# Performance work log

Hardware: AMD Instinct MI355X
Metric: run time of the kernel (lower is better)

Reference implementation:

```python
import jax, jax.numpy as jnp
import numpy as np

N = 8192      # num nodes (fea.shape[0])
IN = 512      # in_features (fea.shape[1])
H = 64        # nhidden
DEG = 32      # avg degree
E = N * DEG   # num edges


def setup_inputs() -> dict:
    key = jax.random.key(0)
    k1, k2, k3 = jax.random.split(key, 3)
    x = jax.random.normal(k1, (N, IN), dtype=jnp.float32)
    # glorot-uniform-scaled params (stored as [in, out] for x @ W)
    W = jax.random.uniform(k2, (IN, H), jnp.float32, -1.0, 1.0) * np.sqrt(6.0 / (IN + H))
    a = jax.random.uniform(k3, (2 * H, 1), jnp.float32, -1.0, 1.0) * np.sqrt(6.0 / (2 * H + 1))
    # structured edge list: no self-loops, no duplicate edges (matches nonzero of a
    # zero-diagonal adjacency; indexed-assignment scatter then has unique targets)
    src = jnp.repeat(jnp.arange(N, dtype=jnp.int32), DEG)
    offs = jnp.tile(jnp.arange(1, DEG + 1, dtype=jnp.int32), N)
    dst = (src + offs) % N
    edge_index = jnp.stack([src, dst])  # [2, E]
    return {"x": x, "W": W, "a": a, "edge_index": edge_index}


def reference(x, W, a, edge_index):
    src, dst = edge_index[0], edge_index[1]
    n = x.shape[0]
    h = a.shape[0] // 2
    Wx = x @ W                                   # [N, H]
    # cat(fea1, fea2) @ a  ==  fea1 @ a[:h] + fea2 @ a[h:]
    e = (Wx @ a[:h])[src, 0] + (Wx @ a[h:])[dst, 0]   # [E]
    coef = jnp.exp(jax.nn.leaky_relu(e, negative_slope=0.1))
    # dense scatter into NxN adjacency (faithful to original)
    A = jnp.zeros((n, n), dtype=x.dtype).at[src, dst].set(coef)
    s1 = A.sum(axis=1)
    # rows with zero sum get a 1 on the diagonal (diag is 0 there, so add == set)
    diag = jnp.arange(n)
    A = A.at[diag, diag].add(jnp.where(s1 == 0, jnp.float32(1.0), jnp.float32(0.0)))
    # (A.t() / A.sum(1)).t()  ==  row-normalize
    return A / A.sum(axis=1, keepdims=True)
```

## Files before the change

### kernel.cpp

```cpp
#include <hip/hip_runtime.h>

#define N_NODES 8192
#define IN_F    512
#define NH      64

__global__ void k_prep(const float* __restrict__ W, const float* __restrict__ a,
                       float* __restrict__ wa1, float* __restrict__ wa2) {
    int tid = blockIdx.x * blockDim.x + threadIdx.x;
    if (tid < IN_F) {
        const float* wrow = W + tid * NH;
        float d1 = 0.f, d2 = 0.f;
#pragma unroll
        for (int k = 0; k < NH; ++k) {
            float w = wrow[k];
            d1 += w * a[k];
            d2 += w * a[NH + k];
        }
        wa1[tid] = d1;
        wa2[tid] = d2;
    }
}

__global__ void k_scores(const float* __restrict__ x, const float* __restrict__ wa1,
                         const float* __restrict__ wa2, float* __restrict__ s1,
                         float* __restrict__ s2) {
    int gid  = blockIdx.x * blockDim.x + threadIdx.x;
    int node = gid >> 6;
    int lane = threadIdx.x & 63;
    if (node >= N_NODES) return;
    const float4* xr = (const float4*)(x + (size_t)node * IN_F);
    const float4* w1 = (const float4*)wa1;
    const float4* w2 = (const float4*)wa2;
    float d1 = 0.f, d2 = 0.f;
#pragma unroll
    for (int i = 0; i < 2; ++i) {
        int idx = lane + 64 * i;
        float4 xv = xr[idx];
        float4 a1 = w1[idx];
        float4 a2 = w2[idx];
        d1 += xv.x * a1.x + xv.y * a1.y + xv.z * a1.z + xv.w * a1.w;
        d2 += xv.x * a2.x + xv.y * a2.y + xv.z * a2.z + xv.w * a2.w;
    }
#pragma unroll
    for (int off = 32; off > 0; off >>= 1) {
        d1 += __shfl_xor(d1, off, 64);
        d2 += __shfl_xor(d2, off, 64);
    }
    if (lane == 0) { s1[node] = d1; s2[node] = d2; }
}

__global__ __launch_bounds__(256)
void k_row(const int* __restrict__ src, const int* __restrict__ dst,
           const float* __restrict__ s1, const float* __restrict__ s2,
           float* __restrict__ out, int deg) {
    const int row = blockIdx.x;
    const int tid = threadIdx.x;
    __shared__ float coefs[256];
    __shared__ int   cols[256];
    __shared__ float rsum_s;

    if (tid < deg) {
        int e  = row * deg + tid;
        int sv = src[e], dv = dst[e];
        float ev = s1[sv] + s2[dv];
        float l  = ev > 0.f ? ev : 0.1f * ev;
        coefs[tid] = __expf(l) == __expf(l) ? expf(l) : expf(l);
        coefs[tid] = expf(l);
        cols[tid]  = (sv == row) ? dv : -1;
    }
    __syncthreads();
    if (tid == 0) {
        float t = 0.f;
        for (int k = 0; k < deg; ++k) t += coefs[k];
        rsum_s = t;
    }
    __syncthreads();
    const float rs = rsum_s;

    float* orf = out + (size_t)row * N_NODES;
    float4* orow = (float4*)orf;
    const float4 z = make_float4(0.f, 0.f, 0.f, 0.f);
#pragma unroll
    for (int i = 0; i < (N_NODES / 4) / 256; ++i)
        orow[tid + 256 * i] = z;
    __syncthreads();

    if (tid < deg && cols[tid] >= 0)
        orf[cols[tid]] = coefs[tid] / rs;
    if (tid == 0 && rs == 0.f)
        orf[row] = 1.0f;
}

extern "C" void kernel_launch(void* const* d_in, const int* in_sizes, int n_in,
                              void* d_out, int out_size, void* d_ws, size_t ws_size,
                              hipStream_t stream) {
    const float* x  = (const float*)d_in[0];
    const float* W  = (const float*)d_in[1];
    const float* a  = (const float*)d_in[2];
    const int*   ei = (const int*)d_in[3];
    const int E = in_sizes[3] / 2;
    const int deg = E / N_NODES;
    const int* src = ei;
    const int* dst = ei + E;

    float* ws  = (float*)d_ws;
    float* wa1 = ws;
    float* wa2 = wa1 + IN_F;
    float* s1  = wa2 + IN_F;
    float* s2  = s1 + N_NODES;

    float* out = (float*)d_out;

    k_prep<<<(IN_F + 255) / 256, 256, 0, stream>>>(W, a, wa1, wa2);
    k_scores<<<(N_NODES * 64) / 256, 256, 0, stream>>>(x, wa1, wa2, s1, s2);
    k_row<<<N_NODES, 256, 0, stream>>>(src, dst, s1, s2, out, deg);
}
```

Baseline: 294.3 us.

## Stage each output row in LDS and stream it out with nontemporal stores

Each block now builds its full adjacency row in shared memory (zeroing, scattering coefficients, setting the diagonal fallback) and then writes the normalized row to global memory once with vectorized nontemporal stores. This removes the separate global zero pass followed by scattered global writes, and folds normalization into the store. The row sum uses a parallel tree reduction and the block size doubles to 512 threads. The cost is 32 KB of LDS per block, which limits how many blocks can be resident per CU.

```diff
diff --git a/kernel.cpp b/kernel.cpp
--- a/kernel.cpp
+++ b/kernel.cpp
@@ -3,6 +3,9 @@
 #define N_NODES 8192
 #define IN_F    512
 #define NH      64
+#define RB      512
+
+typedef float v4f __attribute__((ext_vector_type(4)));
 
 __global__ void k_prep(const float* __restrict__ W, const float* __restrict__ a,
                        float* __restrict__ wa1, float* __restrict__ wa2) {
@@ -49,46 +52,52 @@
     if (lane == 0) { s1[node] = d1; s2[node] = d2; }
 }
 
-__global__ __launch_bounds__(256)
+__global__ __launch_bounds__(RB)
 void k_row(const int* __restrict__ src, const int* __restrict__ dst,
            const float* __restrict__ s1, const float* __restrict__ s2,
            float* __restrict__ out, int deg) {
     const int row = blockIdx.x;
     const int tid = threadIdx.x;
-    __shared__ float coefs[256];
-    __shared__ int   cols[256];
-    __shared__ float rsum_s;
+    __shared__ float rowbuf[N_NODES];
+    __shared__ float csum[RB];
 
+    v4f* rb4 = (v4f*)rowbuf;
+    const v4f z = {0.f, 0.f, 0.f, 0.f};
+#pragma unroll
+    for (int i = 0; i < (N_NODES / 4) / RB; ++i)
+        rb4[tid + RB * i] = z;
+
+    float c = 0.f;
+    int col = -1;
     if (tid < deg) {
         int e  = row * deg + tid;
         int sv = src[e], dv = dst[e];
         float ev = s1[sv] + s2[dv];
         float l  = ev > 0.f ? ev : 0.1f * ev;
-        coefs[tid] = __expf(l) == __expf(l) ? expf(l) : expf(l);
-        coefs[tid] = expf(l);
-        cols[tid]  = (sv == row) ? dv : -1;
+        c = expf(l);
+        if (sv == row) col = dv;
     }
+    csum[tid] = c;
     __syncthreads();
-    if (tid == 0) {
-        float t = 0.f;
-        for (int k = 0; k < deg; ++k) t += coefs[k];
-        rsum_s = t;
+    if (col >= 0) rowbuf[col] = c;
+
+    for (int s = RB / 2; s > 0; s >>= 1) {
+        if (tid < s) csum[tid] += csum[tid + s];
+        __syncthreads();
     }
+    const float rs = csum[0];
+    if (tid == 0 && rs == 0.f) rowbuf[row] = 1.0f;
     __syncthreads();
-    const float rs = rsum_s;
+    const float inv = (rs == 0.f) ? 1.0f : 1.0f / rs;
 
-    float* orf = out + (size_t)row * N_NODES;
-    float4* orow = (float4*)orf;
-    const float4 z = make_float4(0.f, 0.f, 0.f, 0.f);
+    v4f* orow4 = (v4f*)(out + (size_t)row * N_NODES);
 #pragma unroll
-    for (int i = 0; i < (N_NODES / 4) / 256; ++i)
-        orow[tid + 256 * i] = z;
-    __syncthreads();
-
-    if (tid < deg && cols[tid] >= 0)
-        orf[cols[tid]] = coefs[tid] / rs;
-    if (tid == 0 && rs == 0.f)
-        orf[row] = 1.0f;
+    for (int i = 0; i < (N_NODES / 4) / RB; ++i) {
+        int idx = tid + RB * i;
+        v4f v = rb4[idx];
+        v *= inv;
+        __builtin_nontemporal_store(v, &orow4[idx]);
+    }
 }
 
 extern "C" void kernel_launch(void* const* d_in, const int* in_sizes, int n_in,
@@ -113,5 +122,5 @@
 
     k_prep<<<(IN_F + 255) / 256, 256, 0, stream>>>(W, a, wa1, wa2);
     k_scores<<<(N_NODES * 64) / 256, 256, 0, stream>>>(x, wa1, wa2, s1, s2);
-    k_row<<<N_NODES, 256, 0, stream>>>(src, dst, s1, s2, out, deg);
+    k_row<<<N_NODES, RB, 0, stream>>>(src, dst, s1, s2, out, deg);
 }
```

Result: faster. 286.0 us (-2.8%).
